# Performance work log

Hardware: AMD Instinct MI355X
Metric: run time of the kernel (lower is better)

Reference implementation:

```python
import jax, jax.numpy as jnp
import numpy as np
from jax import lax

L, D, S, T, BATCH, NC = 4, 256, 64, 2048, 64, 10
EPS = 1e-5


def setup_inputs() -> dict:
    key = jax.random.key(0)
    ks = iter(jax.random.split(key, 16))
    n = lambda shape, s=1.0: jax.random.normal(next(ks), shape, dtype=jnp.float32) * s
    return {
        "x": n((BATCH, 1, T)),
        "emb_w": n((D, 1), 0.1), "emb_b": jnp.zeros((D,), jnp.float32),
        "Am": n((L, S, S), 0.01), "Bm": n((L, S, D), 0.01),
        "Cm": n((L, D, S), 0.01), "Dm": n((L, D, D), 0.01),
        "in_w": n((L, D, D), 0.05), "in_b": jnp.zeros((L, D), jnp.float32),
        "out_w": n((L, D, D), 0.05), "out_b": jnp.zeros((L, D), jnp.float32),
        "s4ln_w": jnp.ones((L, D), jnp.float32), "s4ln_b": jnp.zeros((L, D), jnp.float32),
        "ln_w": jnp.ones((L, D), jnp.float32), "ln_b": jnp.zeros((L, D), jnp.float32),
        "c1_w": n((512, D), 0.05), "c1_b": jnp.zeros((512,), jnp.float32),
        "bn1_g": jnp.ones((512,), jnp.float32), "bn1_b": jnp.zeros((512,), jnp.float32),
        "bn1_m": jnp.zeros((512,), jnp.float32), "bn1_v": jnp.ones((512,), jnp.float32),
        "c2_w": n((256, 512), 0.05), "c2_b": jnp.zeros((256,), jnp.float32),
        "bn2_g": jnp.ones((256,), jnp.float32), "bn2_b": jnp.zeros((256,), jnp.float32),
        "bn2_m": jnp.zeros((256,), jnp.float32), "bn2_v": jnp.ones((256,), jnp.float32),
        "c3_w": n((NC, 256), 0.05), "c3_b": jnp.zeros((NC,), jnp.float32),
    }


def _ln(x, w, b):
    m = jnp.mean(x, axis=-1, keepdims=True)
    v = jnp.mean((x - m) ** 2, axis=-1, keepdims=True)
    return (x - m) * lax.rsqrt(v + EPS) * w + b


def reference(x, emb_w, emb_b, Am, Bm, Cm, Dm, in_w, in_b, out_w, out_b,
              s4ln_w, s4ln_b, ln_w, ln_b, c1_w, c1_b, bn1_g, bn1_b, bn1_m, bn1_v,
              c2_w, c2_b, bn2_g, bn2_b, bn2_m, bn2_v, c3_w, c3_b):
    # x: (B, 1, T) -> (B, T, 1) -> embed to (B, T, D)
    h = jnp.transpose(x, (0, 2, 1)) @ emb_w.T + emb_b
    Bsz = h.shape[0]
    for l in range(L):
        res = h
        u = _ln(h @ in_w[l].T + in_b[l], s4ln_w[l], s4ln_b[l])  # input_proj + norm
        # precompute time-invariant input drives: (T, B, S) and (T, B, D)
        uB = jnp.einsum('btd,sd->tbs', u, Bm[l])
        uD = jnp.einsum('btd,ed->tbe', u, Dm[l])
        A = Am[l]

        def step(s, ub):  # s_t = s_{t-1} @ A^T + x_t @ B^T
            s = s @ A.T + ub
            return s, s

        _, hs = lax.scan(step, jnp.zeros((Bsz, S), h.dtype), uB)  # hs: (T, B, S)
        y = jnp.einsum('tbs,ds->btd', hs, Cm[l]) + jnp.transpose(uD, (1, 0, 2))
        y = y @ out_w[l].T + out_b[l]  # output_proj (dropout = identity in eval)
        h = _ln(y + res, ln_w[l], ln_b[l])  # residual + outer LayerNorm
    pooled = jnp.mean(h, axis=1)  # AdaptiveAvgPool1d(1) over time -> (B, D)
    z = pooled @ c1_w.T + c1_b
    z = jax.nn.relu((z - bn1_m) * lax.rsqrt(bn1_v + EPS) * bn1_g + bn1_b)
    z = z @ c2_w.T + c2_b
    z = jax.nn.relu((z - bn2_m) * lax.rsqrt(bn2_v + EPS) * bn2_g + bn2_b)
    return z @ c3_w.T + c3_b
```

## Files before the change

### kernel.cpp

```cpp
#include <hip/hip_runtime.h>


#define EPSF 1e-5f

typedef _Float16 F16;
typedef _Float16 half8 __attribute__((ext_vector_type(8)));
typedef float f32x4 __attribute__((ext_vector_type(4)));

constexpr int  Bc  = 64;
constexpr int  Tc  = 2048;
constexpr int  Dc  = 256;
constexpr int  Sc  = 64;
constexpr int  Lc  = 4;
constexpr int  KC  = 12;
constexpr int  NCc = 10;
constexpr int  PAD = 16;
constexpr long BT  = (long)Bc * Tc;
constexpr int  TPB = Tc + PAD;

constexpr size_t OFF_H16  = 0;
constexpr size_t OFF_U16  = OFF_H16 + (size_t)BT * Dc * 2;
constexpr size_t OFF_UBP  = OFF_U16 + (size_t)BT * Dc * 2;
constexpr size_t OFF_S16  = OFF_UBP + (size_t)Bc * TPB * Sc * 2;
constexpr size_t OFF_T16  = OFF_S16 + (size_t)BT * Sc * 2;
constexpr size_t OFF_IW16 = OFF_T16 + (size_t)Lc * KC * Sc * Sc * 2;
constexpr size_t OFF_OW16 = OFF_IW16 + (size_t)Lc * Dc * Dc * 2;
constexpr size_t OFF_BM16 = OFF_OW16 + (size_t)Lc * Dc * Dc * 2;
constexpr size_t OFF_CM16 = OFF_BM16 + (size_t)Lc * Sc * Dc * 2;
constexpr size_t OFF_DM16 = OFF_CM16 + (size_t)Lc * Dc * Sc * 2;
constexpr size_t OFF_PP   = OFF_DM16 + (size_t)Lc * Dc * Dc * 2;
constexpr size_t WS_NEED  = OFF_PP + (size_t)Bc * 32 * Dc * 4;

#define MFMA16(a, b, c) __builtin_amdgcn_mfma_f32_16x16x32_f16((a), (b), (c), 0, 0, 0)

__global__ __launch_bounds__(256) void diag_kernel(float* __restrict__ outp,
                                                   int n, float wsmb)
{
    int i = blockIdx.x * 256 + threadIdx.x;
    if (i < n) outp[i] = (i == 0) ? wsmb : 0.f;
}

__global__ __launch_bounds__(256) void cvt16_kernel(
    const float* __restrict__ src, F16* __restrict__ dst)
{
    long i = ((long)blockIdx.x * 256 + threadIdx.x) * 8;
    float4 a = *(const float4*)(src + i);
    float4 b = *(const float4*)(src + i + 4);
    half8 h;
    h[0] = (F16)a.x; h[1] = (F16)a.y; h[2] = (F16)a.z; h[3] = (F16)a.w;
    h[4] = (F16)b.x; h[5] = (F16)b.y; h[6] = (F16)b.z; h[7] = (F16)b.w;
    *(half8*)(dst + i) = h;
}

__global__ __launch_bounds__(256) void embed_kernel(
    const float* __restrict__ x, const float* __restrict__ ew,
    const float* __restrict__ eb, F16* __restrict__ h16)
{
    long i = ((long)blockIdx.x * 256 + threadIdx.x) * 8;
    int d = (int)(i & 255);
    long bt = i >> 8;
    float xv = x[bt];
    float4 w0 = *(const float4*)(ew + d), w1 = *(const float4*)(ew + d + 4);
    float4 b0 = *(const float4*)(eb + d), b1 = *(const float4*)(eb + d + 4);
    half8 h;
    h[0] = (F16)fmaf(xv, w0.x, b0.x); h[1] = (F16)fmaf(xv, w0.y, b0.y);
    h[2] = (F16)fmaf(xv, w0.z, b0.z); h[3] = (F16)fmaf(xv, w0.w, b0.w);
    h[4] = (F16)fmaf(xv, w1.x, b1.x); h[5] = (F16)fmaf(xv, w1.y, b1.y);
    h[6] = (F16)fmaf(xv, w1.z, b1.z); h[7] = (F16)fmaf(xv, w1.w, b1.w);
    *(half8*)(h16 + i) = h;
}

__global__ __launch_bounds__(256) void apow_kernel(
    const float* __restrict__ Am, F16* __restrict__ taps)
{
    int l = blockIdx.x;
    const float* A = Am + (long)l * Sc * Sc;
    F16* out = taps + (long)l * KC * Sc * Sc;
    __shared__ float sA[64][68];
    __shared__ float sP[64][68];
    int tid = threadIdx.x;

    for (int idx = tid; idx < 64 * 16; idx += 256) {
        int r = idx >> 4, q = idx & 15;
        float4 v = *(const float4*)(A + r * 64 + q * 4);
        *(float4*)&sA[r][q * 4] = v;
        float4 id;
        id.x = (q * 4 + 0 == r) ? 1.f : 0.f;
        id.y = (q * 4 + 1 == r) ? 1.f : 0.f;
        id.z = (q * 4 + 2 == r) ? 1.f : 0.f;
        id.w = (q * 4 + 3 == r) ? 1.f : 0.f;
        *(float4*)&sP[r][q * 4] = id;
        out[r * 64 + q * 4 + 0] = (F16)id.x;
        out[r * 64 + q * 4 + 1] = (F16)id.y;
        out[r * 64 + q * 4 + 2] = (F16)id.z;
        out[r * 64 + q * 4 + 3] = (F16)id.w;
    }
    __syncthreads();

    int rb = (tid >> 4) * 4;
    int cb = (tid & 15) * 4;
    for (int k = 1; k < KC; ++k) {
        float nacc[4][4];
#pragma unroll
        for (int i = 0; i < 4; i++)
#pragma unroll
            for (int u = 0; u < 4; u++) nacc[i][u] = 0.f;
        for (int s = 0; s < 64; ++s) {
            float4 p = *(const float4*)&sP[s][cb];
#pragma unroll
            for (int i = 0; i < 4; i++) {
                float a = sA[rb + i][s];
                nacc[i][0] = fmaf(a, p.x, nacc[i][0]);
                nacc[i][1] = fmaf(a, p.y, nacc[i][1]);
                nacc[i][2] = fmaf(a, p.z, nacc[i][2]);
                nacc[i][3] = fmaf(a, p.w, nacc[i][3]);
            }
        }
        __syncthreads();
#pragma unroll
        for (int i = 0; i < 4; i++) {
            *(float4*)&sP[rb + i][cb] = make_float4(nacc[i][0], nacc[i][1], nacc[i][2], nacc[i][3]);
#pragma unroll
            for (int c = 0; c < 4; c++)
                out[(long)k * 4096 + (rb + i) * 64 + cb + c] = (F16)nacc[i][c];
        }
        __syncthreads();
    }
}

__global__ __launch_bounds__(256) void zeropad_kernel(F16* __restrict__ ubp)
{
    long i8 = ((long)blockIdx.x * 256 + threadIdx.x) * 8;
    int b = (int)(i8 >> 10);
    int off = (int)(i8 & 1023);
    *(uint4*)(ubp + (long)b * TPB * Sc + off) = make_uint4(0u, 0u, 0u, 0u);
}

template<int DIR>
__global__ __launch_bounds__(1024) void mfma_gemm_ln_kernel(
    const F16* X, F16* out, const F16* __restrict__ W,
    const float* __restrict__ bias,
    const float* __restrict__ lnw, const float* __restrict__ lnb)
{
    __shared__ half8 sW[16 * 8 * 64];
    __shared__ float sLN[2][256][2];
    const int tid = threadIdx.x;
    const int lane = tid & 63, wv = tid >> 6;
    const int r15 = lane & 15, hi4 = lane >> 4;
    const int mgrp = wv >> 1, nhalf = wv & 1;
    const int nb = nhalf * 8;

#pragma unroll
    for (int it = 0; it < 8; ++it) {
        int fid = tid + it * 1024;
        int l2 = fid & 63, pair = fid >> 6;
        int n = pair >> 3, ks = pair & 7;
        sW[fid] = *(const half8*)(W + (n * 16 + (l2 & 15)) * Dc + ks * 32 + (l2 >> 4) * 8);
    }
    __syncthreads();

    const long m0 = (long)blockIdx.x * 256 + mgrp * 32;

    f32x4 acc[2][8];
#pragma unroll
    for (int r2 = 0; r2 < 2; ++r2)
#pragma unroll
        for (int n = 0; n < 8; ++n) acc[r2][n] = f32x4{0.f, 0.f, 0.f, 0.f};

    const F16* xb = X + (m0 + r15) * Dc + (hi4 << 3);

    for (int ks = 0; ks < 8; ++ks) {
        half8 a0 = *(const half8*)(xb + ks * 32);
        half8 a1 = *(const half8*)(xb + 16 * Dc + ks * 32);
#pragma unroll
        for (int n = 0; n < 8; ++n) {
            half8 b = sW[((nb + n) * 8 + ks) * 64 + lane];
            acc[0][n] = MFMA16(a0, b, acc[0][n]);
            acc[1][n] = MFMA16(a1, b, acc[1][n]);
        }
    }

    float psum[2][4], pssq[2][4];
#pragma unroll
    for (int r2 = 0; r2 < 2; ++r2)
#pragma unroll
        for (int r = 0; r < 4; ++r) { psum[r2][r] = 0.f; pssq[r2][r] = 0.f; }

#pragma unroll
    for (int r2 = 0; r2 < 2; ++r2) {
        const long rowb = m0 + r2 * 16 + hi4 * 4;
#pragma unroll
        for (int n = 0; n < 8; ++n) {
            float bv = bias[(nb + n) * 16 + r15];
#pragma unroll
            for (int r = 0; r < 4; ++r) {
                float v = acc[r2][n][r] + bv;
                if (DIR) v += (float)out[(rowb + r) * Dc + (nb + n) * 16 + r15];
                acc[r2][n][r] = v;
                psum[r2][r] += v;
                pssq[r2][r] = fmaf(v, v, pssq[r2][r]);
            }
        }
    }
#pragma unroll
    for (int r2 = 0; r2 < 2; ++r2)
#pragma unroll
        for (int r = 0; r < 4; ++r) {
#pragma unroll
            for (int m = 1; m < 16; m <<= 1) {
                psum[r2][r] += __shfl_xor(psum[r2][r], m);
                pssq[r2][r] += __shfl_xor(pssq[r2][r], m);
            }
        }
    if (r15 == 0) {
#pragma unroll
        for (int r2 = 0; r2 < 2; ++r2)
#pragma unroll
            for (int r = 0; r < 4; ++r) {
                int row = mgrp * 32 + r2 * 16 + hi4 * 4 + r;
                sLN[nhalf][row][0] = psum[r2][r];
                sLN[nhalf][row][1] = pssq[r2][r];
            }
    }
    __syncthreads();

    float lw[8], lb[8];
#pragma unroll
    for (int n = 0; n < 8; ++n) {
        int c = (nb + n) * 16 + r15;
        lw[n] = lnw[c]; lb[n] = lnb[c];
    }
#pragma unroll
    for (int r2 = 0; r2 < 2; ++r2) {
        const long rowb = m0 + r2 * 16 + hi4 * 4;
#pragma unroll
        for (int r = 0; r < 4; ++r) {
            int row = mgrp * 32 + r2 * 16 + hi4 * 4 + r;
            float s = sLN[0][row][0] + sLN[1][row][0];
            float q = sLN[0][row][1] + sLN[1][row][1];
            float mean = s * (1.f / 256.f);
            float var  = fmaf(-mean, mean, q * (1.f / 256.f));
            float rs   = rsqrtf(var + EPSF);
#pragma unroll
            for (int n = 0; n < 8; ++n) {
                float val = fmaf((acc[r2][n][r] - mean) * rs, lw[n], lb[n]);
                out[(rowb + r) * Dc + (nb + n) * 16 + r15] = (F16)val;
            }
        }
    }
}

__global__ __launch_bounds__(1024) void mfma_ub_kernel(
    const F16* __restrict__ X, const F16* __restrict__ W, F16* __restrict__ UBP)
{
    __shared__ half8 sW[4 * 8 * 64];
    const int tid = threadIdx.x;
    const int lane = tid & 63, wv = tid >> 6;
    const int r15 = lane & 15, hi4 = lane >> 4;

#pragma unroll
    for (int it = 0; it < 2; ++it) {
        int fid = tid + it * 1024;
        int l2 = fid & 63, pair = fid >> 6;
        int n = pair >> 3, ks = pair & 7;
        sW[fid] = *(const half8*)(W + (n * 16 + (l2 & 15)) * Dc + ks * 32 + (l2 >> 4) * 8);
    }
    __syncthreads();

    const long m0 = (long)blockIdx.x * 512 + wv * 32;
    const long b  = m0 >> 11;
    const long tl = m0 & (Tc - 1);

    f32x4 acc[2][4];
#pragma unroll
    for (int r2 = 0; r2 < 2; ++r2)
#pragma unroll
        for (int n = 0; n < 4; ++n) acc[r2][n] = f32x4{0.f, 0.f, 0.f, 0.f};

    const F16* xb = X + (m0 + r15) * Dc + (hi4 << 3);

    for (int ks = 0; ks < 8; ++ks) {
        half8 a0 = *(const half8*)(xb + ks * 32);
        half8 a1 = *(const half8*)(xb + 16 * Dc + ks * 32);
#pragma unroll
        for (int n = 0; n < 4; ++n) {
            half8 bfr = sW[(n * 8 + ks) * 64 + lane];
            acc[0][n] = MFMA16(a0, bfr, acc[0][n]);
            acc[1][n] = MFMA16(a1, bfr, acc[1][n]);
        }
    }

#pragma unroll
    for (int r2 = 0; r2 < 2; ++r2) {
        const long rowb = b * TPB + PAD + tl + r2 * 16 + hi4 * 4;
#pragma unroll
        for (int n = 0; n < 4; ++n)
#pragma unroll
            for (int r = 0; r < 4; ++r)
                UBP[(rowb + r) * Sc + n * 16 + r15] = (F16)acc[r2][n][r];
    }
}

__global__ __launch_bounds__(1024) void mfma_conv_kernel(
    const F16* __restrict__ UBP, const F16* __restrict__ T16, F16* __restrict__ S16)
{
    __shared__ half8 sT[12 * 4 * 2 * 64];
    const int tid = threadIdx.x;
    const int lane = tid & 63, wv = tid >> 6;
    const int r15 = lane & 15, hi4 = lane >> 4;

#pragma unroll
    for (int it = 0; it < 6; ++it) {
        int fid = tid + it * 1024;
        int l2 = fid & 63, rest = fid >> 6;
        int k = rest >> 3, nk = rest & 7;
        int n = nk >> 1, ks = nk & 1;
        sT[fid] = *(const half8*)(T16 + (long)k * 4096 +
                                  (n * 16 + (l2 & 15)) * Sc + ks * 32 + (l2 >> 4) * 8);
    }
    __syncthreads();

    const long m0 = (long)blockIdx.x * 512 + wv * 32;
    const long b  = m0 >> 11;
    const long tl = m0 & (Tc - 1);

    f32x4 acc[2][4];
#pragma unroll
    for (int r2 = 0; r2 < 2; ++r2)
#pragma unroll
        for (int n = 0; n < 4; ++n) acc[r2][n] = f32x4{0.f, 0.f, 0.f, 0.f};

    const long abase = (b * TPB + PAD + tl + r15) * Sc + (hi4 << 3);

    for (int k = 0; k < KC; ++k) {
        const F16* ap = UBP + abase - (long)k * Sc;
#pragma unroll
        for (int ks = 0; ks < 2; ++ks) {
            half8 a0 = *(const half8*)(ap + ks * 32);
            half8 a1 = *(const half8*)(ap + 16 * Sc + ks * 32);
#pragma unroll
            for (int n = 0; n < 4; ++n) {
                half8 bfr = sT[(k * 8 + n * 2 + ks) * 64 + lane];
                acc[0][n] = MFMA16(a0, bfr, acc[0][n]);
                acc[1][n] = MFMA16(a1, bfr, acc[1][n]);
            }
        }
    }

#pragma unroll
    for (int r2 = 0; r2 < 2; ++r2) {
        const long rowb = m0 + r2 * 16 + hi4 * 4;
#pragma unroll
        for (int n = 0; n < 4; ++n)
#pragma unroll
            for (int r = 0; r < 4; ++r)
                S16[(rowb + r) * Sc + n * 16 + r15] = (F16)acc[r2][n][r];
    }
}

__global__ __launch_bounds__(1024) void mfma_k4_kernel(
    const F16* __restrict__ S16, const F16* __restrict__ C16,
    const F16* U16, const F16* __restrict__ D16, F16* Y16)
{
    __shared__ half8 sD[16 * 8 * 64];
    const int tid = threadIdx.x;
    const int lane = tid & 63, wv = tid >> 6;
    const int r15 = lane & 15, hi4 = lane >> 4;
    const int mgrp = wv >> 1, nhalf = wv & 1;
    const int nb = nhalf * 8;

#pragma unroll
    for (int it = 0; it < 8; ++it) {
        int fid = tid + it * 1024;
        int l2 = fid & 63, pair = fid >> 6;
        int n = pair >> 3, ks = pair & 7;
        sD[fid] = *(const half8*)(D16 + (n * 16 + (l2 & 15)) * Dc + ks * 32 + (l2 >> 4) * 8);
    }
    __syncthreads();

    const long m0 = (long)blockIdx.x * 256 + mgrp * 32;

    f32x4 acc[2][8];
#pragma unroll
    for (int r2 = 0; r2 < 2; ++r2)
#pragma unroll
        for (int n = 0; n < 8; ++n) acc[r2][n] = f32x4{0.f, 0.f, 0.f, 0.f};

    const F16* sb = S16 + (m0 + r15) * Sc + (hi4 << 3);
    const F16* cw = C16 + (long)r15 * Sc + (hi4 << 3);
#pragma unroll
    for (int ks = 0; ks < 2; ++ks) {
        half8 a0 = *(const half8*)(sb + ks * 32);
        half8 a1 = *(const half8*)(sb + 16 * Sc + ks * 32);
#pragma unroll
        for (int n = 0; n < 8; ++n) {
            half8 bfr = *(const half8*)(cw + (nb + n) * 16 * Sc + ks * 32);
            acc[0][n] = MFMA16(a0, bfr, acc[0][n]);
            acc[1][n] = MFMA16(a1, bfr, acc[1][n]);
        }
    }

    const F16* ub = U16 + (m0 + r15) * Dc + (hi4 << 3);
    for (int ks = 0; ks < 8; ++ks) {
        half8 a0 = *(const half8*)(ub + ks * 32);
        half8 a1 = *(const half8*)(ub + 16 * Dc + ks * 32);
#pragma unroll
        for (int n = 0; n < 8; ++n) {
            half8 bfr = sD[((nb + n) * 8 + ks) * 64 + lane];
            acc[0][n] = MFMA16(a0, bfr, acc[0][n]);
            acc[1][n] = MFMA16(a1, bfr, acc[1][n]);
        }
    }

    __syncthreads();

#pragma unroll
    for (int r2 = 0; r2 < 2; ++r2) {
        const long rowb = m0 + r2 * 16 + hi4 * 4;
#pragma unroll
        for (int n = 0; n < 8; ++n)
#pragma unroll
            for (int r = 0; r < 4; ++r)
                Y16[(rowb + r) * Dc + (nb + n) * 16 + r15] = (F16)acc[r2][n][r];
    }
}

__global__ __launch_bounds__(256) void pool_partial_kernel(
    const F16* __restrict__ h16, float* __restrict__ pp)
{
    int b = blockIdx.x >> 5, ch = blockIdx.x & 31;
    const F16* base = h16 + ((long)b * Tc + ch * 64) * Dc + threadIdx.x;
    float s = 0.f;
#pragma unroll 8
    for (int t = 0; t < 64; ++t) s += (float)base[(long)t * Dc];
    pp[((long)b * 32 + ch) * Dc + threadIdx.x] = s;
}

__global__ __launch_bounds__(256) void head_kernel(
    const float* __restrict__ pp,
    const float* __restrict__ c1w, const float* __restrict__ c1b,
    const float* __restrict__ g1, const float* __restrict__ b1,
    const float* __restrict__ m1, const float* __restrict__ v1,
    const float* __restrict__ c2w, const float* __restrict__ c2b,
    const float* __restrict__ g2, const float* __restrict__ b2,
    const float* __restrict__ m2, const float* __restrict__ v2,
    const float* __restrict__ c3w, const float* __restrict__ c3b,
    float* __restrict__ outp)
{
    __shared__ float p[256];
    __shared__ float z1[512];
    __shared__ float z2[256];
    const int b = blockIdx.x, tid = threadIdx.x;

    float s = 0.f;
#pragma unroll
    for (int ch = 0; ch < 32; ++ch) s += pp[((long)b * 32 + ch) * Dc + tid];
    p[tid] = s * (1.f / (float)Tc);
    __syncthreads();

#pragma unroll
    for (int rep = 0; rep < 2; ++rep) {
        int n = tid + rep * 256;
        const float* wr = c1w + (long)n * 256;
        float dot = 0.f;
        for (int k4 = 0; k4 < 64; ++k4) {
            float4 wv = *(const float4*)(wr + k4 * 4);
            float4 pv = *(const float4*)&p[k4 * 4];
            dot = fmaf(wv.x, pv.x, dot);
            dot = fmaf(wv.y, pv.y, dot);
            dot = fmaf(wv.z, pv.z, dot);
            dot = fmaf(wv.w, pv.w, dot);
        }
        float z = (dot + c1b[n] - m1[n]) * rsqrtf(v1[n] + EPSF) * g1[n] + b1[n];
        z1[n] = fmaxf(z, 0.f);
    }
    __syncthreads();

    {
        int n = tid;
        const float* wr = c2w + (long)n * 512;
        float dot = 0.f;
        for (int k4 = 0; k4 < 128; ++k4) {
            float4 wv = *(const float4*)(wr + k4 * 4);
            float4 zv = *(const float4*)&z1[k4 * 4];
            dot = fmaf(wv.x, zv.x, dot);
            dot = fmaf(wv.y, zv.y, dot);
            dot = fmaf(wv.z, zv.z, dot);
            dot = fmaf(wv.w, zv.w, dot);
        }
        float z = (dot + c2b[n] - m2[n]) * rsqrtf(v2[n] + EPSF) * g2[n] + b2[n];
        z2[n] = fmaxf(z, 0.f);
    }
    __syncthreads();

    if (tid < NCc) {
        const float* wr = c3w + (long)tid * 256;
        float dot = 0.f;
        for (int k4 = 0; k4 < 64; ++k4) {
            float4 wv = *(const float4*)(wr + k4 * 4);
            float4 zv = *(const float4*)&z2[k4 * 4];
            dot = fmaf(wv.x, zv.x, dot);
            dot = fmaf(wv.y, zv.y, dot);
            dot = fmaf(wv.z, zv.z, dot);
            dot = fmaf(wv.w, zv.w, dot);
        }
        outp[b * NCc + tid] = dot + c3b[tid];
    }
}

extern "C" void kernel_launch(void* const* d_in, const int* in_sizes, int n_in,
                              void* d_out, int out_size, void* d_ws, size_t ws_size,
                              hipStream_t stream)
{
    float* outp = (float*)d_out;

    if (ws_size < WS_NEED) {
        float wsmb = (float)((double)ws_size / (1024.0 * 1024.0));
        diag_kernel<<<(out_size + 255) / 256, 256, 0, stream>>>(outp, out_size, wsmb);
        return;
    }

    const float* x      = (const float*)d_in[0];
    const float* emb_w  = (const float*)d_in[1];
    const float* emb_b  = (const float*)d_in[2];
    const float* Am     = (const float*)d_in[3];
    const float* Bm     = (const float*)d_in[4];
    const float* Cm     = (const float*)d_in[5];
    const float* Dm     = (const float*)d_in[6];
    const float* in_w   = (const float*)d_in[7];
    const float* in_b   = (const float*)d_in[8];
    const float* out_w  = (const float*)d_in[9];
    const float* out_b  = (const float*)d_in[10];
    const float* s4ln_w = (const float*)d_in[11];
    const float* s4ln_b = (const float*)d_in[12];
    const float* ln_w   = (const float*)d_in[13];
    const float* ln_b   = (const float*)d_in[14];
    const float* c1_w   = (const float*)d_in[15];
    const float* c1_b   = (const float*)d_in[16];
    const float* bn1_g  = (const float*)d_in[17];
    const float* bn1_b  = (const float*)d_in[18];
    const float* bn1_m  = (const float*)d_in[19];
    const float* bn1_v  = (const float*)d_in[20];
    const float* c2_w   = (const float*)d_in[21];
    const float* c2_b   = (const float*)d_in[22];
    const float* bn2_g  = (const float*)d_in[23];
    const float* bn2_b  = (const float*)d_in[24];
    const float* bn2_m  = (const float*)d_in[25];
    const float* bn2_v  = (const float*)d_in[26];
    const float* c3_w   = (const float*)d_in[27];
    const float* c3_b   = (const float*)d_in[28];

    char* wsb = (char*)d_ws;
    F16*   h16  = (F16*)(wsb + OFF_H16);
    F16*   u16  = (F16*)(wsb + OFF_U16);
    F16*   ubp  = (F16*)(wsb + OFF_UBP);
    F16*   s16  = (F16*)(wsb + OFF_S16);
    F16*   t16  = (F16*)(wsb + OFF_T16);
    F16*   iw16 = (F16*)(wsb + OFF_IW16);
    F16*   ow16 = (F16*)(wsb + OFF_OW16);
    F16*   bm16 = (F16*)(wsb + OFF_BM16);
    F16*   cm16 = (F16*)(wsb + OFF_CM16);
    F16*   dm16 = (F16*)(wsb + OFF_DM16);
    float* pp   = (float*)(wsb + OFF_PP);

    const int GB256 = (int)(BT / 256);
    const int GB512 = (int)(BT / 512);

    cvt16_kernel<<<Lc * Dc * Dc / 2048, 256, 0, stream>>>(in_w, iw16);
    cvt16_kernel<<<Lc * Dc * Dc / 2048, 256, 0, stream>>>(out_w, ow16);
    cvt16_kernel<<<Lc * Sc * Dc / 2048, 256, 0, stream>>>(Bm, bm16);
    cvt16_kernel<<<Lc * Dc * Sc / 2048, 256, 0, stream>>>(Cm, cm16);
    cvt16_kernel<<<Lc * Dc * Dc / 2048, 256, 0, stream>>>(Dm, dm16);
    apow_kernel<<<Lc, 256, 0, stream>>>(Am, t16);
    zeropad_kernel<<<32, 256, 0, stream>>>(ubp);
    embed_kernel<<<(int)(BT * Dc / 2048), 256, 0, stream>>>(x, emb_w, emb_b, h16);

    for (int l = 0; l < Lc; ++l) {
        mfma_gemm_ln_kernel<0><<<GB256, 1024, 0, stream>>>(
            h16, u16, iw16 + (long)l * Dc * Dc, in_b + l * Dc,
            s4ln_w + l * Dc, s4ln_b + l * Dc);
        mfma_ub_kernel<<<GB512, 1024, 0, stream>>>(
            u16, bm16 + (long)l * Sc * Dc, ubp);
        mfma_conv_kernel<<<GB512, 1024, 0, stream>>>(
            ubp, t16 + (long)l * KC * Sc * Sc, s16);
        mfma_k4_kernel<<<GB256, 1024, 0, stream>>>(
            s16, cm16 + (long)l * Dc * Sc, u16, dm16 + (long)l * Dc * Dc, u16);
        mfma_gemm_ln_kernel<1><<<GB256, 1024, 0, stream>>>(
            u16, h16, ow16 + (long)l * Dc * Dc, out_b + l * Dc,
            ln_w + l * Dc, ln_b + l * Dc);
    }

    pool_partial_kernel<<<Bc * 32, 256, 0, stream>>>(h16, pp);
    head_kernel<<<Bc, 256, 0, stream>>>(pp,
        c1_w, c1_b, bn1_g, bn1_b, bn1_m, bn1_v,
        c2_w, c2_b, bn2_g, bn2_b, bn2_m, bn2_v,
        c3_w, c3_b, outp);
}
```

Before: 1.070 ms.

## Fuse uB projection into input-proj LN kernel and stage outputs through swizzled LDS

Removes the separate mfma_ub_kernel by computing the u@Bm^T projection inside the input-projection+LayerNorm kernel, reusing the normalized tile already held in shared memory instead of re-reading u16 from global memory. All GEMM epilogues (gemm_ln, conv, k4) now write results into an XOR-swizzled LDS tile and then emit coalesced 16-byte stores, and the residual read in the output LN kernel is likewise staged through LDS. This trades extra barriers and LDS traffic for fewer global passes, one fewer launch per layer, and better-coalesced writes. The Bm fragments in the fused path are read directly from global memory rather than from shared memory.

```diff
diff --git a/kernel.cpp b/kernel.cpp
--- a/kernel.cpp
+++ b/kernel.cpp
@@ -32,6 +32,13 @@
 constexpr size_t WS_NEED  = OFF_PP + (size_t)Bc * 32 * Dc * 4;
 
 #define MFMA16(a, b, c) __builtin_amdgcn_mfma_f32_16x16x32_f16((a), (b), (c), 0, 0, 0)
+
+__device__ __forceinline__ int swz512(int row, int colByte) {
+    return (row * 512 + colByte) ^ ((row & 7) << 4);
+}
+__device__ __forceinline__ int swz128(int row, int colByte) {
+    return (row * 128 + colByte) ^ ((row & 7) << 4);
+}
 
 __global__ __launch_bounds__(256) void diag_kernel(float* __restrict__ outp,
                                                    int n, float wsmb)
@@ -140,15 +147,19 @@
 __global__ __launch_bounds__(1024) void mfma_gemm_ln_kernel(
     const F16* X, F16* out, const F16* __restrict__ W,
     const float* __restrict__ bias,
-    const float* __restrict__ lnw, const float* __restrict__ lnb)
+    const float* __restrict__ lnw, const float* __restrict__ lnb,
+    const F16* __restrict__ Bw, F16* __restrict__ UBP)
 {
     __shared__ half8 sW[16 * 8 * 64];
     __shared__ float sLN[2][256][2];
+    char* bnc = (char*)sW;
+
     const int tid = threadIdx.x;
     const int lane = tid & 63, wv = tid >> 6;
     const int r15 = lane & 15, hi4 = lane >> 4;
     const int mgrp = wv >> 1, nhalf = wv & 1;
     const int nb = nhalf * 8;
+    const long m0g = (long)blockIdx.x * 256;
 
 #pragma unroll
     for (int it = 0; it < 8; ++it) {
@@ -159,7 +170,7 @@
     }
     __syncthreads();
 
-    const long m0 = (long)blockIdx.x * 256 + mgrp * 32;
+    const long m0 = m0g + mgrp * 32;
 
     f32x4 acc[2][8];
 #pragma unroll
@@ -179,6 +190,18 @@
             acc[1][n] = MFMA16(a1, b, acc[1][n]);
         }
     }
+    __syncthreads();
+
+    if (DIR) {
+#pragma unroll
+        for (int it = 0; it < 8; ++it) {
+            int fid = tid + it * 1024;
+            int row = fid >> 5, c8 = fid & 31;
+            half8 v = *(const half8*)(out + (m0g + row) * Dc + c8 * 8);
+            *(half8*)(bnc + swz512(row, c8 * 16)) = v;
+        }
+        __syncthreads();
+    }
 
     float psum[2][4], pssq[2][4];
 #pragma unroll
@@ -188,14 +211,15 @@
 
 #pragma unroll
     for (int r2 = 0; r2 < 2; ++r2) {
-        const long rowb = m0 + r2 * 16 + hi4 * 4;
 #pragma unroll
         for (int n = 0; n < 8; ++n) {
             float bv = bias[(nb + n) * 16 + r15];
+            int colB = ((nb + n) * 16 + r15) * 2;
 #pragma unroll
             for (int r = 0; r < 4; ++r) {
+                int rowloc = mgrp * 32 + r2 * 16 + hi4 * 4 + r;
                 float v = acc[r2][n][r] + bv;
-                if (DIR) v += (float)out[(rowb + r) * Dc + (nb + n) * 16 + r15];
+                if (DIR) v += (float)*(const F16*)(bnc + swz512(rowloc, colB));
                 acc[r2][n][r] = v;
                 psum[r2][r] += v;
                 pssq[r2][r] = fmaf(v, v, pssq[r2][r]);
@@ -224,15 +248,8 @@
     }
     __syncthreads();
 
-    float lw[8], lb[8];
-#pragma unroll
-    for (int n = 0; n < 8; ++n) {
-        int c = (nb + n) * 16 + r15;
-        lw[n] = lnw[c]; lb[n] = lnb[c];
-    }
 #pragma unroll
     for (int r2 = 0; r2 < 2; ++r2) {
-        const long rowb = m0 + r2 * 16 + hi4 * 4;
 #pragma unroll
         for (int r = 0; r < 4; ++r) {
             int row = mgrp * 32 + r2 * 16 + hi4 * 4 + r;
@@ -243,71 +260,67 @@
             float rs   = rsqrtf(var + EPSF);
 #pragma unroll
             for (int n = 0; n < 8; ++n) {
-                float val = fmaf((acc[r2][n][r] - mean) * rs, lw[n], lb[n]);
-                out[(rowb + r) * Dc + (nb + n) * 16 + r15] = (F16)val;
-            }
-        }
-    }
-}
-
-__global__ __launch_bounds__(1024) void mfma_ub_kernel(
-    const F16* __restrict__ X, const F16* __restrict__ W, F16* __restrict__ UBP)
-{
-    __shared__ half8 sW[4 * 8 * 64];
+                int c = (nb + n) * 16 + r15;
+                float val = fmaf((acc[r2][n][r] - mean) * rs, lnw[c], lnb[c]);
+                *(F16*)(bnc + swz512(row, c * 2)) = (F16)val;
+            }
+        }
+    }
+    __syncthreads();
+
+#pragma unroll
+    for (int it = 0; it < 8; ++it) {
+        int fid = tid + it * 1024;
+        int row = fid >> 5, c8 = fid & 31;
+        half8 v = *(const half8*)(bnc + swz512(row, c8 * 16));
+        *(half8*)(out + (m0g + row) * Dc + c8 * 8) = v;
+    }
+
+    if (DIR == 0) {
+        const int mgrp2 = wv >> 1, nh2 = wv & 1;
+        const int row0 = mgrp2 * 32 + r15;
+
+        f32x4 au[2][2];
+#pragma unroll
+        for (int r2 = 0; r2 < 2; ++r2)
+#pragma unroll
+            for (int n = 0; n < 2; ++n) au[r2][n] = f32x4{0.f, 0.f, 0.f, 0.f};
+
+        for (int ks = 0; ks < 8; ++ks) {
+            half8 a0 = *(const half8*)(bnc + swz512(row0,      hi4 * 16 + ks * 64));
+            half8 a1 = *(const half8*)(bnc + swz512(row0 + 16, hi4 * 16 + ks * 64));
+#pragma unroll
+            for (int n = 0; n < 2; ++n) {
+                half8 b = *(const half8*)(Bw + ((nh2 * 2 + n) * 16 + r15) * Dc
+                                          + (hi4 << 3) + ks * 32);
+                au[0][n] = MFMA16(a0, b, au[0][n]);
+                au[1][n] = MFMA16(a1, b, au[1][n]);
+            }
+        }
+
+        const long bb = m0g >> 11;
+        const long tl = m0g & (Tc - 1);
+#pragma unroll
+        for (int r2 = 0; r2 < 2; ++r2) {
+            const long rowb = bb * TPB + PAD + tl + mgrp2 * 32 + r2 * 16 + hi4 * 4;
+#pragma unroll
+            for (int n = 0; n < 2; ++n)
+#pragma unroll
+                for (int r = 0; r < 4; ++r)
+                    UBP[(rowb + r) * Sc + (nh2 * 2 + n) * 16 + r15] = (F16)au[r2][n][r];
+        }
+    }
+}
+
+__global__ __launch_bounds__(1024) void mfma_conv_kernel(
+    const F16* __restrict__ UBP, const F16* __restrict__ T16, F16* __restrict__ S16)
+{
+    __shared__ half8 sT[12 * 4 * 2 * 64];
+    char* bnc = (char*)sT;
     const int tid = threadIdx.x;
     const int lane = tid & 63, wv = tid >> 6;
     const int r15 = lane & 15, hi4 = lane >> 4;
-
-#pragma unroll
-    for (int it = 0; it < 2; ++it) {
-        int fid = tid + it * 1024;
-        int l2 = fid & 63, pair = fid >> 6;
-        int n = pair >> 3, ks = pair & 7;
-        sW[fid] = *(const half8*)(W + (n * 16 + (l2 & 15)) * Dc + ks * 32 + (l2 >> 4) * 8);
-    }
-    __syncthreads();
-
-    const long m0 = (long)blockIdx.x * 512 + wv * 32;
-    const long b  = m0 >> 11;
-    const long tl = m0 & (Tc - 1);
-
-    f32x4 acc[2][4];
-#pragma unroll
-    for (int r2 = 0; r2 < 2; ++r2)
-#pragma unroll
-        for (int n = 0; n < 4; ++n) acc[r2][n] = f32x4{0.f, 0.f, 0.f, 0.f};
-
-    const F16* xb = X + (m0 + r15) * Dc + (hi4 << 3);
-
-    for (int ks = 0; ks < 8; ++ks) {
-        half8 a0 = *(const half8*)(xb + ks * 32);
-        half8 a1 = *(const half8*)(xb + 16 * Dc + ks * 32);
-#pragma unroll
-        for (int n = 0; n < 4; ++n) {
-            half8 bfr = sW[(n * 8 + ks) * 64 + lane];
-            acc[0][n] = MFMA16(a0, bfr, acc[0][n]);
-            acc[1][n] = MFMA16(a1, bfr, acc[1][n]);
-        }
-    }
-
-#pragma unroll
-    for (int r2 = 0; r2 < 2; ++r2) {
-        const long rowb = b * TPB + PAD + tl + r2 * 16 + hi4 * 4;
-#pragma unroll
-        for (int n = 0; n < 4; ++n)
-#pragma unroll
-            for (int r = 0; r < 4; ++r)
-                UBP[(rowb + r) * Sc + n * 16 + r15] = (F16)acc[r2][n][r];
-    }
-}
-
-__global__ __launch_bounds__(1024) void mfma_conv_kernel(
-    const F16* __restrict__ UBP, const F16* __restrict__ T16, F16* __restrict__ S16)
-{
-    __shared__ half8 sT[12 * 4 * 2 * 64];
-    const int tid = threadIdx.x;
-    const int lane = tid & 63, wv = tid >> 6;
-    const int r15 = lane & 15, hi4 = lane >> 4;
+    const long m0g = (long)blockIdx.x * 512;
 
 #pragma unroll
     for (int it = 0; it < 6; ++it) {
@@ -320,7 +333,7 @@
     }
     __syncthreads();
 
-    const long m0 = (long)blockIdx.x * 512 + wv * 32;
+    const long m0 = m0g + wv * 32;
     const long b  = m0 >> 11;
     const long tl = m0 & (Tc - 1);
 
@@ -346,15 +359,26 @@
             }
         }
     }
+    __syncthreads();
 
 #pragma unroll
     for (int r2 = 0; r2 < 2; ++r2) {
-        const long rowb = m0 + r2 * 16 + hi4 * 4;
 #pragma unroll
         for (int n = 0; n < 4; ++n)
 #pragma unroll
-            for (int r = 0; r < 4; ++r)
-                S16[(rowb + r) * Sc + n * 16 + r15] = (F16)acc[r2][n][r];
+            for (int r = 0; r < 4; ++r) {
+                int row = wv * 32 + r2 * 16 + hi4 * 4 + r;
+                *(F16*)(bnc + swz128(row, (n * 16 + r15) * 2)) = (F16)acc[r2][n][r];
+            }
+    }
+    __syncthreads();
+
+#pragma unroll
+    for (int it = 0; it < 4; ++it) {
+        int fid = tid + it * 1024;
+        int row = fid >> 3, c8 = fid & 7;
+        half8 v = *(const half8*)(bnc + swz128(row, c8 * 16));
+        *(half8*)(S16 + (m0g + row) * Sc + c8 * 8) = v;
     }
 }
 
@@ -363,11 +387,13 @@
     const F16* U16, const F16* __restrict__ D16, F16* Y16)
 {
     __shared__ half8 sD[16 * 8 * 64];
+    char* bnc = (char*)sD;
     const int tid = threadIdx.x;
     const int lane = tid & 63, wv = tid >> 6;
     const int r15 = lane & 15, hi4 = lane >> 4;
     const int mgrp = wv >> 1, nhalf = wv & 1;
     const int nb = nhalf * 8;
+    const long m0g = (long)blockIdx.x * 256;
 
 #pragma unroll
     for (int it = 0; it < 8; ++it) {
@@ -378,7 +404,7 @@
     }
     __syncthreads();
 
-    const long m0 = (long)blockIdx.x * 256 + mgrp * 32;
+    const long m0 = m0g + mgrp * 32;
 
     f32x4 acc[2][8];
 #pragma unroll
@@ -411,17 +437,26 @@
             acc[1][n] = MFMA16(a1, bfr, acc[1][n]);
         }
     }
-
     __syncthreads();
 
 #pragma unroll
     for (int r2 = 0; r2 < 2; ++r2) {
-        const long rowb = m0 + r2 * 16 + hi4 * 4;
 #pragma unroll
         for (int n = 0; n < 8; ++n)
 #pragma unroll
-            for (int r = 0; r < 4; ++r)
-                Y16[(rowb + r) * Dc + (nb + n) * 16 + r15] = (F16)acc[r2][n][r];
+            for (int r = 0; r < 4; ++r) {
+                int row = mgrp * 32 + r2 * 16 + hi4 * 4 + r;
+                *(F16*)(bnc + swz512(row, ((nb + n) * 16 + r15) * 2)) = (F16)acc[r2][n][r];
+            }
+    }
+    __syncthreads();
+
+#pragma unroll
+    for (int it = 0; it < 8; ++it) {
+        int fid = tid + it * 1024;
+        int row = fid >> 5, c8 = fid & 31;
+        half8 v = *(const half8*)(bnc + swz512(row, c8 * 16));
+        *(half8*)(Y16 + (m0g + row) * Dc + c8 * 8) = v;
     }
 }
 
@@ -578,16 +613,15 @@
     for (int l = 0; l < Lc; ++l) {
         mfma_gemm_ln_kernel<0><<<GB256, 1024, 0, stream>>>(
             h16, u16, iw16 + (long)l * Dc * Dc, in_b + l * Dc,
-            s4ln_w + l * Dc, s4ln_b + l * Dc);
-        mfma_ub_kernel<<<GB512, 1024, 0, stream>>>(
-            u16, bm16 + (long)l * Sc * Dc, ubp);
+            s4ln_w + l * Dc, s4ln_b + l * Dc,
+            bm16 + (long)l * Sc * Dc, ubp);
         mfma_conv_kernel<<<GB512, 1024, 0, stream>>>(
             ubp, t16 + (long)l * KC * Sc * Sc, s16);
         mfma_k4_kernel<<<GB256, 1024, 0, stream>>>(
             s16, cm16 + (long)l * Dc * Sc, u16, dm16 + (long)l * Dc * Dc, u16);
         mfma_gemm_ln_kernel<1><<<GB256, 1024, 0, stream>>>(
             u16, h16, ow16 + (long)l * Dc * Dc, out_b + l * Dc,
-            ln_w + l * Dc, ln_b + l * Dc);
+            ln_w + l * Dc, ln_b + l * Dc, nullptr, nullptr);
     }
 
     pool_partial_kernel<<<Bc * 32, 256, 0, stream>>>(h16, pp);
```

Result: slower. 1.348 ms (+26.0%).
